# Kernel tuning notes

Hardware: AMD Instinct MI355X
Metric: run time of the kernel (lower is better)

Reference implementation:

```python
import jax, jax.numpy as jnp
import numpy as np
from jax import lax

T, B, D, H, C = 2048, 64, 128, 256, 5

def setup_inputs() -> dict:
    key = jax.random.key(0)
    k = jax.random.split(key, 7)
    s = 1.0 / np.sqrt(H)  # pytorch nn.RNN init scale
    return {
        "inputs": jax.random.normal(k[0], (T, B, D), dtype=jnp.float32),
        "W_ih": jax.random.uniform(k[1], (H, D), jnp.float32, -s, s),
        "W_hh": jax.random.uniform(k[2], (H, H), jnp.float32, -s, s),
        "b_ih": jax.random.uniform(k[3], (H,), jnp.float32, -s, s),
        "b_hh": jax.random.uniform(k[4], (H,), jnp.float32, -s, s),
        "W_fc": jax.random.uniform(k[5], (C, H), jnp.float32, -s, s),
        "b_fc": jax.random.uniform(k[6], (C,), jnp.float32, -s, s),
    }

def reference(inputs, W_ih, W_hh, b_ih, b_hh, W_fc, b_fc):
    # Precompute input projections for all timesteps: (T, B, H)
    x_proj = jnp.einsum('tbd,hd->tbh', inputs, W_ih) + b_ih + b_hh

    def step(h, xp):
        # h_t = tanh(W_ih x_t + b_ih + W_hh h_{t-1} + b_hh)
        h_new = jnp.tanh(xp + h @ W_hh.T)
        return h_new, None  # per-step outputs unused by the module head

    h0 = jnp.zeros((inputs.shape[1], W_hh.shape[0]), dtype=inputs.dtype)
    h_last, _ = lax.scan(step, h0, x_proj)

    logits = h_last @ W_fc.T + b_fc  # (B, 5)
    return jax.nn.log_softmax(logits, axis=1)
```

## Files before the change

### kernel.cpp

```cpp
#include <hip/hip_runtime.h>


#define T_DIM 2048
#define B_DIM 64
#define D_DIM 128
#define H_DIM 256
#define C_DIM 5

using floatx4 = __attribute__((ext_vector_type(4))) float;
using shortx8 = __attribute__((ext_vector_type(8))) short;

#define W_SCALE 2032.0f
#define H_SCALE 127.0f
#define INV_SCALE (1.0f / (2032.0f * 127.0f))
#define TWO_LOG2E 2.8853900817779268f
#define K_EXP (TWO_LOG2E * INV_SCALE)
#define MAGIC 12582912.0f

__device__ __forceinline__ short f2bf(float f) {
  unsigned int u = __float_as_uint(f);
  unsigned int r = (u + 0x7FFFu + ((u >> 16) & 1u)) >> 16;
  return (short)r;
}

__device__ __forceinline__ int sdot4(unsigned int a, unsigned int b, int c) {
#if __has_builtin(__builtin_amdgcn_sdot4)
  return __builtin_amdgcn_sdot4((int)a, (int)b, c, false);
#else
  int r = c;
  #pragma unroll
  for (int k = 0; k < 4; ++k)
    r += (int)(signed char)(a >> (8 * k)) * (int)(signed char)(b >> (8 * k));
  return r;
#endif
}

template<int CTRL>
__device__ __forceinline__ int dpp_movi(int x) {
  return __builtin_amdgcn_update_dpp(0, x, CTRL, 0xF, 0xF, true);
}

__device__ __forceinline__ float fast_exp2(float x) {
#if __has_builtin(__builtin_amdgcn_exp2f)
  return __builtin_amdgcn_exp2f(x);
#else
  return __exp2f(x);
#endif
}

__device__ __forceinline__ float fast_rcp(float x) {
#if __has_builtin(__builtin_amdgcn_rcpf)
  return __builtin_amdgcn_rcpf(x);
#else
  return __fdividef(1.0f, x);
#endif
}

__device__ __forceinline__ void barrier_lds_only() {
  asm volatile("s_waitcnt lgkmcnt(0)\n\ts_barrier" ::: "memory");
}

__device__ __forceinline__ void xp_body(
    const float* __restrict__ x,
    const float* __restrict__ W_ih,
    const float* __restrict__ b_ih,
    const float* __restrict__ b_hh,
    _Float16* __restrict__ xp,
    int cnt, int t0, int tstride, short* wlds)
{
  if (cnt <= 0) return;
  const int tid = threadIdx.x;
  {
    const int group = tid >> 2;
    const int sub = tid & 3;
    const int kf = group & 3;
    const int k0 = kf * 32 + sub * 8;
    #pragma unroll
    for (int i = 0; i < 16; ++i) {
      const int n = (group >> 2) * 16 + i;
      const float* src = W_ih + n * D_DIM + k0;
      float4 p0 = *(const float4*)(src);
      float4 p1 = *(const float4*)(src + 4);
      shortx8 v;
      v[0]=f2bf(p0.x); v[1]=f2bf(p0.y); v[2]=f2bf(p0.z); v[3]=f2bf(p0.w);
      v[4]=f2bf(p1.x); v[5]=f2bf(p1.y); v[6]=f2bf(p1.z); v[7]=f2bf(p1.w);
      *(shortx8*)&wlds[(group * 64 + sub * 16 + i) * 8] = v;
    }
  }
  __syncthreads();

  const int wv   = tid >> 6;
  const int lane = tid & 63;
  const int col  = lane & 15;
  const int quad = lane >> 4;

  float bias[16];
  #pragma unroll
  for (int nt = 0; nt < 16; ++nt)
    bias[nt] = b_ih[nt * 16 + col] + b_hh[nt * 16 + col];

  for (int t = t0; t < cnt; t += tstride) {
    const long m0 = (long)t * 64 + wv * 16;

    shortx8 af[4];
    const float* arow = x + (m0 + col) * D_DIM + quad * 8;
    #pragma unroll
    for (int kf = 0; kf < 4; ++kf) {
      float4 p0 = *(const float4*)(arow + kf * 32);
      float4 p1 = *(const float4*)(arow + kf * 32 + 4);
      shortx8 v;
      v[0]=f2bf(p0.x); v[1]=f2bf(p0.y); v[2]=f2bf(p0.z); v[3]=f2bf(p0.w);
      v[4]=f2bf(p1.x); v[5]=f2bf(p1.y); v[6]=f2bf(p1.z); v[7]=f2bf(p1.w);
      af[kf] = v;
    }

    #pragma unroll
    for (int nt = 0; nt < 16; ++nt) {
      floatx4 acc = {0.f, 0.f, 0.f, 0.f};
      #pragma unroll
      for (int kf = 0; kf < 4; ++kf) {
        shortx8 bfrag = *(const shortx8*)&wlds[((nt * 4 + kf) * 64 + lane) * 8];
        acc = __builtin_amdgcn_mfma_f32_16x16x32_bf16(af[kf], bfrag, acc, 0, 0, 0);
      }
      const int n = nt * 16 + col;
      #pragma unroll
      for (int r = 0; r < 4; ++r) {
        const long m = m0 + quad * 4 + r;
        xp[m * H_DIM + n] = (_Float16)(acc[r] + bias[nt]);
      }
    }
  }
}

__global__ __launch_bounds__(256) void xp_kernel(
    const float* __restrict__ x, const float* __restrict__ W_ih,
    const float* __restrict__ b_ih, const float* __restrict__ b_hh,
    _Float16* __restrict__ xp, int cnt)
{
  __shared__ __align__(16) short wlds[32768];
  xp_body(x, W_ih, b_ih, b_hh, xp, cnt, blockIdx.x, gridDim.x, wlds);
}

__global__ __launch_bounds__(256)
__attribute__((amdgpu_waves_per_eu(1, 1)))
void fused_kernel(
    const _Float16* __restrict__ xp,
    const float* __restrict__ W_hh,
    const float* __restrict__ W_fc,
    const float* __restrict__ b_fc,
    signed char* __restrict__ h8,
    float* __restrict__ out,
    int cnt, int first, int last,
    const float* __restrict__ x_next,
    const float* __restrict__ W_ih,
    const float* __restrict__ b_ih,
    const float* __restrict__ b_hh,
    _Float16* __restrict__ xp_next,
    int next_cnt)
{
  __shared__ __align__(16) short wlds[32768];
  __shared__ __align__(16) signed char hbuf[2][256];
  __shared__ float hfin[H_DIM];
  __shared__ float scratch[192];

  if (blockIdx.x >= 64) {
    xp_body(x_next, W_ih, b_ih, b_hh, xp_next, next_cnt,
            (int)blockIdx.x - 64, (int)gridDim.x - 64, wlds);
    return;
  }

  const int b   = blockIdx.x;
  const int tid = threadIdx.x;
  const int g   = tid >> 2;
  const int c   = tid & 3;

  unsigned int wq[4][16];
  const float* wbase = W_hh + (g * 4) * H_DIM + c * 64;
  #pragma unroll
  for (int r = 0; r < 4; ++r)
    #pragma unroll
    for (int i = 0; i < 16; ++i) {
      float4 f = *(const float4*)(wbase + r * H_DIM + i * 4);
      unsigned int q0 = (unsigned int)(int)rintf(f.x * W_SCALE) & 0xFFu;
      unsigned int q1 = (unsigned int)(int)rintf(f.y * W_SCALE) & 0xFFu;
      unsigned int q2 = (unsigned int)(int)rintf(f.z * W_SCALE) & 0xFFu;
      unsigned int q3 = (unsigned int)(int)rintf(f.w * W_SCALE) & 0xFFu;
      wq[r][i] = q0 | (q1 << 8) | (q2 << 16) | (q3 << 24);
    }
  #pragma unroll
  for (int r = 0; r < 4; ++r)
    #pragma unroll
    for (int i = 0; i < 16; ++i)
      asm volatile("" : "+v"(wq[r][i]));

  const int row_w = tid;
  hbuf[0][row_w] = first ? (signed char)0 : h8[b * H_DIM + row_w];
  __syncthreads();

  const size_t BH = (size_t)B_DIM * H_DIM;
  const _Float16* xpp = xp + (size_t)b * H_DIM + row_w;
  float hnlast = 0.f;

  auto step_body = [&](int bufsel, _Float16 xin) -> void {
    float xin2 = (float)xin * TWO_LOG2E;
    const signed char* hb = hbuf[bufsel] + c * 64;
    uint4 u0 = *(const uint4*)(hb);
    uint4 u1 = *(const uint4*)(hb + 16);
    uint4 u2 = *(const uint4*)(hb + 32);
    uint4 u3 = *(const uint4*)(hb + 48);
    const unsigned int hv[16] = {u0.x, u0.y, u0.z, u0.w, u1.x, u1.y, u1.z, u1.w,
                                 u2.x, u2.y, u2.z, u2.w, u3.x, u3.y, u3.z, u3.w};
    int a0l = 0, a1l = 0, a2l = 0, a3l = 0;
    int a0h = 0, a1h = 0, a2h = 0, a3h = 0;
    #pragma unroll
    for (int i = 0; i < 8; ++i) {
      a0l = sdot4(wq[0][i], hv[i], a0l);
      a1l = sdot4(wq[1][i], hv[i], a1l);
      a2l = sdot4(wq[2][i], hv[i], a2l);
      a3l = sdot4(wq[3][i], hv[i], a3l);
    }
    #pragma unroll
    for (int i = 8; i < 16; ++i) {
      a0h = sdot4(wq[0][i], hv[i], a0h);
      a1h = sdot4(wq[1][i], hv[i], a1h);
      a2h = sdot4(wq[2][i], hv[i], a2h);
      a3h = sdot4(wq[3][i], hv[i], a3h);
    }
    int a0 = a0l + a0h, a1 = a1l + a1h, a2 = a2l + a2h, a3 = a3l + a3h;
    int k01 = (c & 1) ? a1 : a0;
    int s01 = (c & 1) ? a0 : a1;
    int m0  = k01 + dpp_movi<0xB1>(s01);
    int k23 = (c & 1) ? a3 : a2;
    int s23 = (c & 1) ? a2 : a3;
    int m1  = k23 + dpp_movi<0xB1>(s23);
    int kk = (c & 2) ? m1 : m0;
    int sn = (c & 2) ? m0 : m1;
    int vi = kk + dpp_movi<0x4E>(sn);

    float arg = __builtin_fmaf((float)vi, K_EXP, xin2);
    float e   = fast_exp2(arg);
    float r   = fast_rcp(e + 1.0f);
    hnlast    = __builtin_fmaf(-254.0f, r, 127.0f);
    float qb  = __builtin_fmaf(-254.0f, r, MAGIC + 127.0f);
    hbuf[bufsel ^ 1][row_w] = (signed char)__float_as_int(qb);
    barrier_lds_only();
  };

  if ((cnt & 1) == 0 && cnt >= 2) {
    const _Float16* p = xpp;
    _Float16 x0 = p[0];
    _Float16 x1 = p[BH];
    for (int s = 0; s + 2 < cnt; s += 2) {
      step_body(0, x0); x0 = p[2 * BH];
      step_body(1, x1); x1 = p[3 * BH];
      p += 2 * BH;
    }
    step_body(0, x0);
    step_body(1, x1);
  } else {
    for (int s = 0; s < cnt; ++s)
      step_body(s & 1, xpp[(size_t)s * BH]);
  }

  h8[b * H_DIM + row_w] = hbuf[cnt & 1][row_w];

  if (last) {
    hfin[row_w] = hnlast * (1.0f / 127.0f);
    __syncthreads();
    if (tid < 160) {
      const int c5 = tid >> 5, i = tid & 31;
      float pp = 0.f;
      #pragma unroll
      for (int jj = 0; jj < 8; ++jj) {
        const int j = i * 8 + jj;
        pp += W_fc[c5 * H_DIM + j] * hfin[j];
      }
      scratch[tid] = pp;
    }
    __syncthreads();
    if (tid < C_DIM) {
      float l = b_fc[tid];
      for (int i = 0; i < 32; ++i) l += scratch[tid * 32 + i];
      scratch[160 + tid] = l;
    }
    __syncthreads();
    if (tid == 0) {
      float mx = scratch[160];
      for (int i = 1; i < C_DIM; ++i) mx = fmaxf(mx, scratch[160 + i]);
      float se = 0.f;
      for (int i = 0; i < C_DIM; ++i) se += __expf(scratch[160 + i] - mx);
      const float lse = mx + __logf(se);
      for (int i = 0; i < C_DIM; ++i) out[b * C_DIM + i] = scratch[160 + i] - lse;
    }
  }
}

extern "C" void kernel_launch(void* const* d_in, const int* in_sizes, int n_in,
                              void* d_out, int out_size, void* d_ws, size_t ws_size,
                              hipStream_t stream) {
  (void)in_sizes; (void)n_in; (void)out_size;
  const float* x    = (const float*)d_in[0];
  const float* W_ih = (const float*)d_in[1];
  const float* W_hh = (const float*)d_in[2];
  const float* b_ih = (const float*)d_in[3];
  const float* b_hh = (const float*)d_in[4];
  const float* W_fc = (const float*)d_in[5];
  const float* b_fc = (const float*)d_in[6];
  float* out = (float*)d_out;

  char* ws = (char*)d_ws;
  signed char* h8 = (signed char*)ws;
  _Float16* bufA = (_Float16*)(ws + 65536);
  const size_t step_bytes = (size_t)B_DIM * H_DIM * sizeof(_Float16);
  const size_t avail = ws_size > 65536 ? ws_size - 65536 : 0;
  const long cap2 = (long)(avail / (2 * step_bytes));

  if (cap2 >= 64) {
    long CAP = cap2 < 512 ? cap2 : 512;
    _Float16* bufB = bufA + (size_t)CAP * B_DIM * H_DIM;
    long bnd[64];
    bnd[0] = 0;
    long c0 = 256; if (c0 > CAP) c0 = CAP; if (c0 > T_DIM) c0 = T_DIM;
    bnd[1] = c0;
    int nc = 1;
    while (bnd[nc] < T_DIM && nc < 62) {
      long nx = bnd[nc] + CAP; if (nx > T_DIM) nx = T_DIM;
      bnd[nc + 1] = nx; ++nc;
    }
    {
      const unsigned gb = (unsigned)(c0 < 512 ? c0 : 512);
      xp_kernel<<<dim3(gb), dim3(256), 0, stream>>>(x, W_ih, b_ih, b_hh, bufA, (int)c0);
    }
    for (int k = 0; k < nc; ++k) {
      _Float16* src = (k & 1) ? bufB : bufA;
      _Float16* dst = (k & 1) ? bufA : bufB;
      const long s0 = bnd[k], s1 = bnd[k + 1];
      const int has_next = (k + 1 < nc) ? 1 : 0;
      const long n0 = has_next ? bnd[k + 1] : 0;
      const long n1 = has_next ? bnd[k + 2] : 0;
      fused_kernel<<<dim3(256), dim3(256), 0, stream>>>(
          src, W_hh, W_fc, b_fc, h8, out,
          (int)(s1 - s0), k == 0 ? 1 : 0, (k == nc - 1) ? 1 : 0,
          x + n0 * B_DIM * D_DIM, W_ih, b_ih, b_hh, dst, (int)(n1 - n0));
    }
  } else {
    long Tc = (long)(avail / step_bytes);
    if (Tc > T_DIM) Tc = T_DIM;
    if (Tc < 1) Tc = 1;
    for (long t0 = 0; t0 < T_DIM; t0 += Tc) {
      const long cnt = (T_DIM - t0 < Tc) ? (T_DIM - t0) : Tc;
      const unsigned gb = (unsigned)(cnt < 512 ? cnt : 512);
      xp_kernel<<<dim3(gb), dim3(256), 0, stream>>>(
          x + t0 * B_DIM * D_DIM, W_ih, b_ih, b_hh, bufA, (int)cnt);
      fused_kernel<<<dim3(64), dim3(256), 0, stream>>>(
          bufA, W_hh, W_fc, b_fc, h8, out,
          (int)cnt, t0 == 0 ? 1 : 0, (t0 + cnt == T_DIM) ? 1 : 0,
          x, W_ih, b_ih, b_hh, bufA, 0);
    }
  }
}
```

Measured before the change: 731.2 us.

## Process two batch rows per recurrent block to amortize barriers

Each recurrent block now handles two independent batch sequences, interleaving their per-step dot products before a single LDS barrier, so the barrier and latency cost per step is shared across two rows and the two chains can hide each other's latency. Recurrent blocks drop from 64 to 32, which frees more CUs for the overlapped input-projection work. The trade-off is roughly twice the serial arithmetic per block per step, which lengthens the critical path if the step was compute-bound rather than latency-bound.

```diff
diff --git a/kernel.cpp b/kernel.cpp
--- a/kernel.cpp
+++ b/kernel.cpp
@@ -159,17 +159,17 @@
     int next_cnt)
 {
   __shared__ __align__(16) short wlds[32768];
-  __shared__ __align__(16) signed char hbuf[2][256];
+  __shared__ __align__(16) signed char hbuf[2][2][256];
   __shared__ float hfin[H_DIM];
   __shared__ float scratch[192];
 
-  if (blockIdx.x >= 64) {
+  if (blockIdx.x >= 32) {
     xp_body(x_next, W_ih, b_ih, b_hh, xp_next, next_cnt,
-            (int)blockIdx.x - 64, (int)gridDim.x - 64, wlds);
+            (int)blockIdx.x - 32, (int)gridDim.x - 32, wlds);
     return;
   }
 
-  const int b   = blockIdx.x;
+  const int b0  = blockIdx.x * 2;
   const int tid = threadIdx.x;
   const int g   = tid >> 2;
   const int c   = tid & 3;
@@ -194,16 +194,18 @@
       asm volatile("" : "+v"(wq[r][i]));
 
   const int row_w = tid;
-  hbuf[0][row_w] = first ? (signed char)0 : h8[b * H_DIM + row_w];
+  hbuf[0][0][row_w] = first ? (signed char)0 : h8[b0 * H_DIM + row_w];
+  hbuf[1][0][row_w] = first ? (signed char)0 : h8[(b0 + 1) * H_DIM + row_w];
   __syncthreads();
 
   const size_t BH = (size_t)B_DIM * H_DIM;
-  const _Float16* xpp = xp + (size_t)b * H_DIM + row_w;
-  float hnlast = 0.f;
-
-  auto step_body = [&](int bufsel, _Float16 xin) -> void {
+  const _Float16* pA = xp + (size_t)b0 * H_DIM + row_w;
+  const _Float16* pB = pA + H_DIM;
+  float hn[2] = {0.f, 0.f};
+
+  auto phase = [&](int bb, int bufsel, _Float16 xin) -> void {
     float xin2 = (float)xin * TWO_LOG2E;
-    const signed char* hb = hbuf[bufsel] + c * 64;
+    const signed char* hb = hbuf[bb][bufsel] + c * 64;
     uint4 u0 = *(const uint4*)(hb);
     uint4 u1 = *(const uint4*)(hb + 16);
     uint4 u2 = *(const uint4*)(hb + 32);
@@ -240,57 +242,72 @@
     float arg = __builtin_fmaf((float)vi, K_EXP, xin2);
     float e   = fast_exp2(arg);
     float r   = fast_rcp(e + 1.0f);
-    hnlast    = __builtin_fmaf(-254.0f, r, 127.0f);
+    hn[bb]    = __builtin_fmaf(-254.0f, r, 127.0f);
     float qb  = __builtin_fmaf(-254.0f, r, MAGIC + 127.0f);
-    hbuf[bufsel ^ 1][row_w] = (signed char)__float_as_int(qb);
+    hbuf[bb][bufsel ^ 1][row_w] = (signed char)__float_as_int(qb);
+  };
+
+  if ((cnt & 1) == 0 && cnt >= 4) {
+    _Float16 xA0 = pA[0];
+    _Float16 xB0 = pB[0];
+    _Float16 xA1 = pA[BH];
+    _Float16 xB1 = pB[BH];
+    for (int s = 0; s + 2 < cnt; s += 2) {
+      phase(0, 0, xA0); phase(1, 0, xB0);
+      barrier_lds_only();
+      xA0 = pA[2 * BH]; xB0 = pB[2 * BH];
+      phase(0, 1, xA1); phase(1, 1, xB1);
+      barrier_lds_only();
+      xA1 = pA[3 * BH]; xB1 = pB[3 * BH];
+      pA += 2 * BH; pB += 2 * BH;
+    }
+    phase(0, 0, xA0); phase(1, 0, xB0);
     barrier_lds_only();
-  };
-
-  if ((cnt & 1) == 0 && cnt >= 2) {
-    const _Float16* p = xpp;
-    _Float16 x0 = p[0];
-    _Float16 x1 = p[BH];
-    for (int s = 0; s + 2 < cnt; s += 2) {
-      step_body(0, x0); x0 = p[2 * BH];
-      step_body(1, x1); x1 = p[3 * BH];
-      p += 2 * BH;
-    }
-    step_body(0, x0);
-    step_body(1, x1);
+    phase(0, 1, xA1); phase(1, 1, xB1);
+    barrier_lds_only();
   } else {
-    for (int s = 0; s < cnt; ++s)
-      step_body(s & 1, xpp[(size_t)s * BH]);
-  }
-
-  h8[b * H_DIM + row_w] = hbuf[cnt & 1][row_w];
+    for (int s = 0; s < cnt; ++s) {
+      phase(0, s & 1, pA[(size_t)s * BH]);
+      phase(1, s & 1, pB[(size_t)s * BH]);
+      barrier_lds_only();
+    }
+  }
+
+  h8[b0 * H_DIM + row_w]       = hbuf[0][cnt & 1][row_w];
+  h8[(b0 + 1) * H_DIM + row_w] = hbuf[1][cnt & 1][row_w];
 
   if (last) {
-    hfin[row_w] = hnlast * (1.0f / 127.0f);
-    __syncthreads();
-    if (tid < 160) {
-      const int c5 = tid >> 5, i = tid & 31;
-      float pp = 0.f;
-      #pragma unroll
-      for (int jj = 0; jj < 8; ++jj) {
-        const int j = i * 8 + jj;
-        pp += W_fc[c5 * H_DIM + j] * hfin[j];
-      }
-      scratch[tid] = pp;
-    }
-    __syncthreads();
-    if (tid < C_DIM) {
-      float l = b_fc[tid];
-      for (int i = 0; i < 32; ++i) l += scratch[tid * 32 + i];
-      scratch[160 + tid] = l;
-    }
-    __syncthreads();
-    if (tid == 0) {
-      float mx = scratch[160];
-      for (int i = 1; i < C_DIM; ++i) mx = fmaxf(mx, scratch[160 + i]);
-      float se = 0.f;
-      for (int i = 0; i < C_DIM; ++i) se += __expf(scratch[160 + i] - mx);
-      const float lse = mx + __logf(se);
-      for (int i = 0; i < C_DIM; ++i) out[b * C_DIM + i] = scratch[160 + i] - lse;
+    #pragma unroll
+    for (int bb = 0; bb < 2; ++bb) {
+      __syncthreads();
+      hfin[row_w] = hn[bb] * (1.0f / 127.0f);
+      __syncthreads();
+      if (tid < 160) {
+        const int c5 = tid >> 5, i = tid & 31;
+        float pp = 0.f;
+        #pragma unroll
+        for (int jj = 0; jj < 8; ++jj) {
+          const int j = i * 8 + jj;
+          pp += W_fc[c5 * H_DIM + j] * hfin[j];
+        }
+        scratch[tid] = pp;
+      }
+      __syncthreads();
+      if (tid < C_DIM) {
+        float l = b_fc[tid];
+        for (int i = 0; i < 32; ++i) l += scratch[tid * 32 + i];
+        scratch[160 + tid] = l;
+      }
+      __syncthreads();
+      if (tid == 0) {
+        float mx = scratch[160];
+        for (int i = 1; i < C_DIM; ++i) mx = fmaxf(mx, scratch[160 + i]);
+        float se = 0.f;
+        for (int i = 0; i < C_DIM; ++i) se += __expf(scratch[160 + i] - mx);
+        const float lse = mx + __logf(se);
+        for (int i = 0; i < C_DIM; ++i)
+          out[(b0 + bb) * C_DIM + i] = scratch[160 + i] - lse;
+      }
     }
   }
 }
@@ -352,7 +369,7 @@
       const unsigned gb = (unsigned)(cnt < 512 ? cnt : 512);
       xp_kernel<<<dim3(gb), dim3(256), 0, stream>>>(
           x + t0 * B_DIM * D_DIM, W_ih, b_ih, b_hh, bufA, (int)cnt);
-      fused_kernel<<<dim3(64), dim3(256), 0, stream>>>(
+      fused_kernel<<<dim3(32), dim3(256), 0, stream>>>(
           bufA, W_hh, W_fc, b_fc, h8, out,
           (int)cnt, t0 == 0 ? 1 : 0, (t0 + cnt == T_DIM) ? 1 : 0,
           x, W_ih, b_ih, b_hh, bufA, 0);
```

Result: slower. 1.189 ms (+62.6%).

## Replace chunked kernel launches with persistent cooperative producer-consumer kernel

Applied to the files above, without the earlier changes.

Replaces the sequence of per-chunk fused launches with a single cooperative persistent kernel. 192 producer blocks compute input projections into a ring buffer and publish per-chunk counters with atomics, while 64 consumer blocks spin on those flags and run the recurrence over 128-step chunks. The aim is to remove repeated launch overhead, repeated W_hh quantisation, and h8 spill/reload between chunks, and to overlap projection work with the scan. The cost is spin-wait polling and fences, and the design depends on cooperative launch co-residency, with the old multi-launch path kept as a fallback.

```diff
diff --git a/kernel.cpp b/kernel.cpp
--- a/kernel.cpp
+++ b/kernel.cpp
@@ -6,12 +6,14 @@
 #define D_DIM 128
 #define H_DIM 256
 #define C_DIM 5
+#define CHUNK 128
+#define NCH   (T_DIM / CHUNK)
+#define NPROD 192
 
 using floatx4 = __attribute__((ext_vector_type(4))) float;
 using shortx8 = __attribute__((ext_vector_type(8))) short;
 
 #define W_SCALE 2032.0f
-#define H_SCALE 127.0f
 #define INV_SCALE (1.0f / (2032.0f * 127.0f))
 #define TWO_LOG2E 2.8853900817779268f
 #define K_EXP (TWO_LOG2E * INV_SCALE)
@@ -60,122 +62,123 @@
   asm volatile("s_waitcnt lgkmcnt(0)\n\ts_barrier" ::: "memory");
 }
 
-__device__ __forceinline__ void xp_body(
-    const float* __restrict__ x,
-    const float* __restrict__ W_ih,
-    const float* __restrict__ b_ih,
-    const float* __restrict__ b_hh,
-    _Float16* __restrict__ xp,
-    int cnt, int t0, int tstride, short* wlds)
+__device__ __forceinline__ void xp_stage_w(const float* __restrict__ W_ih, short* wlds) {
+  const int tid = threadIdx.x;
+  const int group = tid >> 2;
+  const int sub = tid & 3;
+  const int kf = group & 3;
+  const int k0 = kf * 32 + sub * 8;
+  #pragma unroll
+  for (int i = 0; i < 16; ++i) {
+    const int n = (group >> 2) * 16 + i;
+    const float* src = W_ih + n * D_DIM + k0;
+    float4 p0 = *(const float4*)(src);
+    float4 p1 = *(const float4*)(src + 4);
+    shortx8 v;
+    v[0]=f2bf(p0.x); v[1]=f2bf(p0.y); v[2]=f2bf(p0.z); v[3]=f2bf(p0.w);
+    v[4]=f2bf(p1.x); v[5]=f2bf(p1.y); v[6]=f2bf(p1.z); v[7]=f2bf(p1.w);
+    *(shortx8*)&wlds[(group * 64 + sub * 16 + i) * 8] = v;
+  }
+}
+
+__device__ __forceinline__ void xp_one_t(
+    const float* __restrict__ x, const float* bias, const short* wlds,
+    long t, _Float16* __restrict__ dst)
 {
-  if (cnt <= 0) return;
-  const int tid = threadIdx.x;
-  {
-    const int group = tid >> 2;
-    const int sub = tid & 3;
-    const int kf = group & 3;
-    const int k0 = kf * 32 + sub * 8;
-    #pragma unroll
-    for (int i = 0; i < 16; ++i) {
-      const int n = (group >> 2) * 16 + i;
-      const float* src = W_ih + n * D_DIM + k0;
-      float4 p0 = *(const float4*)(src);
-      float4 p1 = *(const float4*)(src + 4);
-      shortx8 v;
-      v[0]=f2bf(p0.x); v[1]=f2bf(p0.y); v[2]=f2bf(p0.z); v[3]=f2bf(p0.w);
-      v[4]=f2bf(p1.x); v[5]=f2bf(p1.y); v[6]=f2bf(p1.z); v[7]=f2bf(p1.w);
-      *(shortx8*)&wlds[(group * 64 + sub * 16 + i) * 8] = v;
-    }
-  }
-  __syncthreads();
-
+  const int tid  = threadIdx.x;
   const int wv   = tid >> 6;
   const int lane = tid & 63;
   const int col  = lane & 15;
   const int quad = lane >> 4;
 
-  float bias[16];
-  #pragma unroll
-  for (int nt = 0; nt < 16; ++nt)
-    bias[nt] = b_ih[nt * 16 + col] + b_hh[nt * 16 + col];
-
-  for (int t = t0; t < cnt; t += tstride) {
-    const long m0 = (long)t * 64 + wv * 16;
-
-    shortx8 af[4];
-    const float* arow = x + (m0 + col) * D_DIM + quad * 8;
+  shortx8 af[4];
+  const float* arow = x + ((size_t)t * B_DIM + wv * 16 + col) * D_DIM + quad * 8;
+  #pragma unroll
+  for (int kf = 0; kf < 4; ++kf) {
+    float4 p0 = *(const float4*)(arow + kf * 32);
+    float4 p1 = *(const float4*)(arow + kf * 32 + 4);
+    shortx8 v;
+    v[0]=f2bf(p0.x); v[1]=f2bf(p0.y); v[2]=f2bf(p0.z); v[3]=f2bf(p0.w);
+    v[4]=f2bf(p1.x); v[5]=f2bf(p1.y); v[6]=f2bf(p1.z); v[7]=f2bf(p1.w);
+    af[kf] = v;
+  }
+
+  #pragma unroll
+  for (int nt = 0; nt < 16; ++nt) {
+    floatx4 acc = {0.f, 0.f, 0.f, 0.f};
     #pragma unroll
     for (int kf = 0; kf < 4; ++kf) {
-      float4 p0 = *(const float4*)(arow + kf * 32);
-      float4 p1 = *(const float4*)(arow + kf * 32 + 4);
-      shortx8 v;
-      v[0]=f2bf(p0.x); v[1]=f2bf(p0.y); v[2]=f2bf(p0.z); v[3]=f2bf(p0.w);
-      v[4]=f2bf(p1.x); v[5]=f2bf(p1.y); v[6]=f2bf(p1.z); v[7]=f2bf(p1.w);
-      af[kf] = v;
-    }
-
-    #pragma unroll
-    for (int nt = 0; nt < 16; ++nt) {
-      floatx4 acc = {0.f, 0.f, 0.f, 0.f};
-      #pragma unroll
-      for (int kf = 0; kf < 4; ++kf) {
-        shortx8 bfrag = *(const shortx8*)&wlds[((nt * 4 + kf) * 64 + lane) * 8];
-        acc = __builtin_amdgcn_mfma_f32_16x16x32_bf16(af[kf], bfrag, acc, 0, 0, 0);
-      }
-      const int n = nt * 16 + col;
-      #pragma unroll
-      for (int r = 0; r < 4; ++r) {
-        const long m = m0 + quad * 4 + r;
-        xp[m * H_DIM + n] = (_Float16)(acc[r] + bias[nt]);
-      }
-    }
-  }
-}
-
-__global__ __launch_bounds__(256) void xp_kernel(
-    const float* __restrict__ x, const float* __restrict__ W_ih,
-    const float* __restrict__ b_ih, const float* __restrict__ b_hh,
-    _Float16* __restrict__ xp, int cnt)
-{
-  __shared__ __align__(16) short wlds[32768];
-  xp_body(x, W_ih, b_ih, b_hh, xp, cnt, blockIdx.x, gridDim.x, wlds);
+      shortx8 bfrag = *(const shortx8*)&wlds[((nt * 4 + kf) * 64 + lane) * 8];
+      acc = __builtin_amdgcn_mfma_f32_16x16x32_bf16(af[kf], bfrag, acc, 0, 0, 0);
+    }
+    const int n = nt * 16 + col;
+    #pragma unroll
+    for (int r = 0; r < 4; ++r) {
+      const int m = wv * 16 + quad * 4 + r;
+      dst[(size_t)m * H_DIM + n] = (_Float16)(acc[r] + bias[nt]);
+    }
+  }
 }
 
 __global__ __launch_bounds__(256)
 __attribute__((amdgpu_waves_per_eu(1, 1)))
-void fused_kernel(
-    const _Float16* __restrict__ xp,
+void rnn_persistent(
+    const float* __restrict__ x,
+    const float* __restrict__ W_ih,
     const float* __restrict__ W_hh,
+    const float* __restrict__ b_ih,
+    const float* __restrict__ b_hh,
     const float* __restrict__ W_fc,
     const float* __restrict__ b_fc,
-    signed char* __restrict__ h8,
+    _Float16* __restrict__ ring,
+    int* __restrict__ flags,
     float* __restrict__ out,
-    int cnt, int first, int last,
-    const float* __restrict__ x_next,
-    const float* __restrict__ W_ih,
-    const float* __restrict__ b_ih,
-    const float* __restrict__ b_hh,
-    _Float16* __restrict__ xp_next,
-    int next_cnt)
+    int R)
 {
   __shared__ __align__(16) short wlds[32768];
   __shared__ __align__(16) signed char hbuf[2][256];
   __shared__ float hfin[H_DIM];
   __shared__ float scratch[192];
 
+  const int tid = threadIdx.x;
+  const size_t BH = (size_t)B_DIM * H_DIM;
+
   if (blockIdx.x >= 64) {
-    xp_body(x_next, W_ih, b_ih, b_hh, xp_next, next_cnt,
-            (int)blockIdx.x - 64, (int)gridDim.x - 64, wlds);
+    xp_stage_w(W_ih, wlds);
+    const int lane = tid & 63, col = lane & 15;
+    float bias[16];
+    #pragma unroll
+    for (int nt = 0; nt < 16; ++nt)
+      bias[nt] = b_ih[nt * 16 + col] + b_hh[nt * 16 + col];
+    __syncthreads();
+
+    const int pidx = (int)blockIdx.x - 64;
+    for (int t = pidx; t < T_DIM; t += NPROD) {
+      const int c = t >> 7;
+      if (c >= R) {
+        if (tid == 0) {
+          while (__hip_atomic_load(&flags[16], __ATOMIC_RELAXED,
+                                   __HIP_MEMORY_SCOPE_AGENT) < 64 * (c - R + 1)) {}
+        }
+        __syncthreads();
+      }
+      _Float16* dst = ring + ((size_t)(c % R) * CHUNK + (t & (CHUNK - 1))) * BH;
+      xp_one_t(x, bias, wlds, t, dst);
+      __threadfence();
+      __syncthreads();
+      if (tid == 0)
+        __hip_atomic_fetch_add(&flags[c], 1, __ATOMIC_RELEASE,
+                               __HIP_MEMORY_SCOPE_AGENT);
+    }
     return;
   }
 
-  const int b   = blockIdx.x;
-  const int tid = threadIdx.x;
-  const int g   = tid >> 2;
-  const int c   = tid & 3;
+  const int b = blockIdx.x;
+  const int g = tid >> 2;
+  const int c4 = tid & 3;
 
   unsigned int wq[4][16];
-  const float* wbase = W_hh + (g * 4) * H_DIM + c * 64;
+  const float* wbase = W_hh + (g * 4) * H_DIM + c4 * 64;
   #pragma unroll
   for (int r = 0; r < 4; ++r)
     #pragma unroll
@@ -194,16 +197,14 @@
       asm volatile("" : "+v"(wq[r][i]));
 
   const int row_w = tid;
-  hbuf[0][row_w] = first ? (signed char)0 : h8[b * H_DIM + row_w];
+  hbuf[0][row_w] = 0;
   __syncthreads();
 
-  const size_t BH = (size_t)B_DIM * H_DIM;
-  const _Float16* xpp = xp + (size_t)b * H_DIM + row_w;
   float hnlast = 0.f;
 
   auto step_body = [&](int bufsel, _Float16 xin) -> void {
-    float xin2 = (float)xin * TWO_LOG2E;
-    const signed char* hb = hbuf[bufsel] + c * 64;
+    float x2 = (float)xin * TWO_LOG2E;
+    const signed char* hb = hbuf[bufsel] + c4 * 64;
     uint4 u0 = *(const uint4*)(hb);
     uint4 u1 = *(const uint4*)(hb + 16);
     uint4 u2 = *(const uint4*)(hb + 32);
@@ -227,17 +228,184 @@
       a3h = sdot4(wq[3][i], hv[i], a3h);
     }
     int a0 = a0l + a0h, a1 = a1l + a1h, a2 = a2l + a2h, a3 = a3l + a3h;
-    int k01 = (c & 1) ? a1 : a0;
-    int s01 = (c & 1) ? a0 : a1;
+    int k01 = (c4 & 1) ? a1 : a0;
+    int s01 = (c4 & 1) ? a0 : a1;
     int m0  = k01 + dpp_movi<0xB1>(s01);
-    int k23 = (c & 1) ? a3 : a2;
-    int s23 = (c & 1) ? a2 : a3;
+    int k23 = (c4 & 1) ? a3 : a2;
+    int s23 = (c4 & 1) ? a2 : a3;
     int m1  = k23 + dpp_movi<0xB1>(s23);
-    int kk = (c & 2) ? m1 : m0;
-    int sn = (c & 2) ? m0 : m1;
+    int kk = (c4 & 2) ? m1 : m0;
+    int sn = (c4 & 2) ? m0 : m1;
     int vi = kk + dpp_movi<0x4E>(sn);
 
-    float arg = __builtin_fmaf((float)vi, K_EXP, xin2);
+    float arg = __builtin_fmaf((float)vi, K_EXP, x2);
+    float e   = fast_exp2(arg);
+    float r   = fast_rcp(e + 1.0f);
+    hnlast    = __builtin_fmaf(-254.0f, r, 127.0f);
+    float qb  = __builtin_fmaf(-254.0f, r, MAGIC + 127.0f);
+    hbuf[bufsel ^ 1][row_w] = (signed char)__float_as_int(qb);
+    barrier_lds_only();
+  };
+
+  for (int c = 0; c < NCH; ++c) {
+    if (tid == 0) {
+      while (__hip_atomic_load(&flags[c], __ATOMIC_RELAXED,
+                               __HIP_MEMORY_SCOPE_AGENT) < CHUNK) {}
+    }
+    __syncthreads();
+    {
+      int fv = __hip_atomic_load(&flags[c], __ATOMIC_ACQUIRE,
+                                 __HIP_MEMORY_SCOPE_AGENT);
+      asm volatile("" :: "v"(fv));
+    }
+
+    const _Float16* p = ring + (size_t)(c % R) * CHUNK * BH
+                             + (size_t)b * H_DIM + row_w;
+    _Float16 x0 = p[0];
+    _Float16 x1 = p[BH];
+    for (int s = 0; s + 2 < CHUNK; s += 2) {
+      step_body(0, x0); x0 = p[2 * BH];
+      step_body(1, x1); x1 = p[3 * BH];
+      p += 2 * BH;
+    }
+    step_body(0, x0);
+    step_body(1, x1);
+
+    if (R < NCH) {
+      __syncthreads();
+      if (tid == 0)
+        __hip_atomic_fetch_add(&flags[16], 1, __ATOMIC_RELAXED,
+                               __HIP_MEMORY_SCOPE_AGENT);
+    }
+  }
+
+  hfin[row_w] = hnlast * (1.0f / 127.0f);
+  __syncthreads();
+  if (tid < 160) {
+    const int c5 = tid >> 5, i = tid & 31;
+    float pp = 0.f;
+    #pragma unroll
+    for (int jj = 0; jj < 8; ++jj) {
+      const int j = i * 8 + jj;
+      pp += W_fc[c5 * H_DIM + j] * hfin[j];
+    }
+    scratch[tid] = pp;
+  }
+  __syncthreads();
+  if (tid < C_DIM) {
+    float l = b_fc[tid];
+    for (int i = 0; i < 32; ++i) l += scratch[tid * 32 + i];
+    scratch[160 + tid] = l;
+  }
+  __syncthreads();
+  if (tid == 0) {
+    float mx = scratch[160];
+    for (int i = 1; i < C_DIM; ++i) mx = fmaxf(mx, scratch[160 + i]);
+    float se = 0.f;
+    for (int i = 0; i < C_DIM; ++i) se += __expf(scratch[160 + i] - mx);
+    const float lse = mx + __logf(se);
+    for (int i = 0; i < C_DIM; ++i) out[b * C_DIM + i] = scratch[160 + i] - lse;
+  }
+}
+
+__global__ __launch_bounds__(256) void xp_fb_kernel(
+    const float* __restrict__ x, const float* __restrict__ W_ih,
+    const float* __restrict__ b_ih, const float* __restrict__ b_hh,
+    _Float16* __restrict__ xp, int cnt)
+{
+  __shared__ __align__(16) short wlds[32768];
+  if (cnt <= 0) return;
+  xp_stage_w(W_ih, wlds);
+  const int col = (threadIdx.x & 63) & 15;
+  float bias[16];
+  #pragma unroll
+  for (int nt = 0; nt < 16; ++nt)
+    bias[nt] = b_ih[nt * 16 + col] + b_hh[nt * 16 + col];
+  __syncthreads();
+  for (int t = blockIdx.x; t < cnt; t += gridDim.x)
+    xp_one_t(x, bias, wlds, t, xp + (size_t)t * B_DIM * H_DIM);
+}
+
+__global__ __launch_bounds__(256)
+__attribute__((amdgpu_waves_per_eu(1, 1)))
+void scan_fb_kernel(
+    const _Float16* __restrict__ xp, const float* __restrict__ W_hh,
+    const float* __restrict__ W_fc, const float* __restrict__ b_fc,
+    signed char* __restrict__ h8, float* __restrict__ out,
+    int cnt, int first, int last)
+{
+  __shared__ __align__(16) signed char hbuf[2][256];
+  __shared__ float hfin[H_DIM];
+  __shared__ float scratch[192];
+  const int b = blockIdx.x;
+  const int tid = threadIdx.x;
+  const int g = tid >> 2;
+  const int c4 = tid & 3;
+
+  unsigned int wq[4][16];
+  const float* wbase = W_hh + (g * 4) * H_DIM + c4 * 64;
+  #pragma unroll
+  for (int r = 0; r < 4; ++r)
+    #pragma unroll
+    for (int i = 0; i < 16; ++i) {
+      float4 f = *(const float4*)(wbase + r * H_DIM + i * 4);
+      unsigned int q0 = (unsigned int)(int)rintf(f.x * W_SCALE) & 0xFFu;
+      unsigned int q1 = (unsigned int)(int)rintf(f.y * W_SCALE) & 0xFFu;
+      unsigned int q2 = (unsigned int)(int)rintf(f.z * W_SCALE) & 0xFFu;
+      unsigned int q3 = (unsigned int)(int)rintf(f.w * W_SCALE) & 0xFFu;
+      wq[r][i] = q0 | (q1 << 8) | (q2 << 16) | (q3 << 24);
+    }
+  #pragma unroll
+  for (int r = 0; r < 4; ++r)
+    #pragma unroll
+    for (int i = 0; i < 16; ++i)
+      asm volatile("" : "+v"(wq[r][i]));
+
+  const int row_w = tid;
+  hbuf[0][row_w] = first ? (signed char)0 : h8[b * H_DIM + row_w];
+  __syncthreads();
+
+  const size_t BH = (size_t)B_DIM * H_DIM;
+  const _Float16* xpp = xp + (size_t)b * H_DIM + row_w;
+  float hnlast = 0.f;
+
+  auto step_body = [&](int bufsel, _Float16 xin) -> void {
+    float x2 = (float)xin * TWO_LOG2E;
+    const signed char* hb = hbuf[bufsel] + c4 * 64;
+    uint4 u0 = *(const uint4*)(hb);
+    uint4 u1 = *(const uint4*)(hb + 16);
+    uint4 u2 = *(const uint4*)(hb + 32);
+    uint4 u3 = *(const uint4*)(hb + 48);
+    const unsigned int hv[16] = {u0.x, u0.y, u0.z, u0.w, u1.x, u1.y, u1.z, u1.w,
+                                 u2.x, u2.y, u2.z, u2.w, u3.x, u3.y, u3.z, u3.w};
+    int a0l = 0, a1l = 0, a2l = 0, a3l = 0;
+    int a0h = 0, a1h = 0, a2h = 0, a3h = 0;
+    #pragma unroll
+    for (int i = 0; i < 8; ++i) {
+      a0l = sdot4(wq[0][i], hv[i], a0l);
+      a1l = sdot4(wq[1][i], hv[i], a1l);
+      a2l = sdot4(wq[2][i], hv[i], a2l);
+      a3l = sdot4(wq[3][i], hv[i], a3l);
+    }
+    #pragma unroll
+    for (int i = 8; i < 16; ++i) {
+      a0h = sdot4(wq[0][i], hv[i], a0h);
+      a1h = sdot4(wq[1][i], hv[i], a1h);
+      a2h = sdot4(wq[2][i], hv[i], a2h);
+      a3h = sdot4(wq[3][i], hv[i], a3h);
+    }
+    int a0 = a0l + a0h, a1 = a1l + a1h, a2 = a2l + a2h, a3 = a3l + a3h;
+    int k01 = (c4 & 1) ? a1 : a0;
+    int s01 = (c4 & 1) ? a0 : a1;
+    int m0  = k01 + dpp_movi<0xB1>(s01);
+    int k23 = (c4 & 1) ? a3 : a2;
+    int s23 = (c4 & 1) ? a2 : a3;
+    int m1  = k23 + dpp_movi<0xB1>(s23);
+    int kk = (c4 & 2) ? m1 : m0;
+    int sn = (c4 & 2) ? m0 : m1;
+    int vi = kk + dpp_movi<0x4E>(sn);
+
+    float arg = __builtin_fmaf((float)vi, K_EXP, x2);
     float e   = fast_exp2(arg);
     float r   = fast_rcp(e + 1.0f);
     hnlast    = __builtin_fmaf(-254.0f, r, 127.0f);
@@ -309,53 +477,39 @@
   float* out = (float*)d_out;
 
   char* ws = (char*)d_ws;
-  signed char* h8 = (signed char*)ws;
-  _Float16* bufA = (_Float16*)(ws + 65536);
+  int* flags = (int*)ws;
+  _Float16* ring = (_Float16*)(ws + 65536);
   const size_t step_bytes = (size_t)B_DIM * H_DIM * sizeof(_Float16);
   const size_t avail = ws_size > 65536 ? ws_size - 65536 : 0;
-  const long cap2 = (long)(avail / (2 * step_bytes));
-
-  if (cap2 >= 64) {
-    long CAP = cap2 < 512 ? cap2 : 512;
-    _Float16* bufB = bufA + (size_t)CAP * B_DIM * H_DIM;
-    long bnd[64];
-    bnd[0] = 0;
-    long c0 = 256; if (c0 > CAP) c0 = CAP; if (c0 > T_DIM) c0 = T_DIM;
-    bnd[1] = c0;
-    int nc = 1;
-    while (bnd[nc] < T_DIM && nc < 62) {
-      long nx = bnd[nc] + CAP; if (nx > T_DIM) nx = T_DIM;
-      bnd[nc + 1] = nx; ++nc;
-    }
-    {
-      const unsigned gb = (unsigned)(c0 < 512 ? c0 : 512);
-      xp_kernel<<<dim3(gb), dim3(256), 0, stream>>>(x, W_ih, b_ih, b_hh, bufA, (int)c0);
-    }
-    for (int k = 0; k < nc; ++k) {
-      _Float16* src = (k & 1) ? bufB : bufA;
-      _Float16* dst = (k & 1) ? bufA : bufB;
-      const long s0 = bnd[k], s1 = bnd[k + 1];
-      const int has_next = (k + 1 < nc) ? 1 : 0;
-      const long n0 = has_next ? bnd[k + 1] : 0;
-      const long n1 = has_next ? bnd[k + 2] : 0;
-      fused_kernel<<<dim3(256), dim3(256), 0, stream>>>(
-          src, W_hh, W_fc, b_fc, h8, out,
-          (int)(s1 - s0), k == 0 ? 1 : 0, (k == nc - 1) ? 1 : 0,
-          x + n0 * B_DIM * D_DIM, W_ih, b_ih, b_hh, dst, (int)(n1 - n0));
-    }
-  } else {
-    long Tc = (long)(avail / step_bytes);
-    if (Tc > T_DIM) Tc = T_DIM;
-    if (Tc < 1) Tc = 1;
-    for (long t0 = 0; t0 < T_DIM; t0 += Tc) {
-      const long cnt = (T_DIM - t0 < Tc) ? (T_DIM - t0) : Tc;
-      const unsigned gb = (unsigned)(cnt < 512 ? cnt : 512);
-      xp_kernel<<<dim3(gb), dim3(256), 0, stream>>>(
-          x + t0 * B_DIM * D_DIM, W_ih, b_ih, b_hh, bufA, (int)cnt);
-      fused_kernel<<<dim3(64), dim3(256), 0, stream>>>(
-          bufA, W_hh, W_fc, b_fc, h8, out,
-          (int)cnt, t0 == 0 ? 1 : 0, (t0 + cnt == T_DIM) ? 1 : 0,
-          x, W_ih, b_ih, b_hh, bufA, 0);
-    }
-  }
-}
+  const long steps = (long)(avail / step_bytes);
+
+  int Rv = (int)(steps / CHUNK);
+  if (Rv > NCH) Rv = NCH;
+
+  if (Rv >= 2) {
+    hipMemsetAsync(ws, 0, 256, stream);
+    void* args[11];
+    args[0] = (void*)&x;    args[1] = (void*)&W_ih; args[2] = (void*)&W_hh;
+    args[3] = (void*)&b_ih; args[4] = (void*)&b_hh; args[5] = (void*)&W_fc;
+    args[6] = (void*)&b_fc; args[7] = (void*)&ring; args[8] = (void*)&flags;
+    args[9] = (void*)&out;  args[10] = (void*)&Rv;
+    hipError_t e = hipLaunchCooperativeKernel(
+        (const void*)rnn_persistent, dim3(256), dim3(256), args, 0, stream);
+    if (e == hipSuccess) return;
+  }
+
+  signed char* h8 = (signed char*)(ws + 4096);
+  long Tc = steps;
+  if (Tc > T_DIM) Tc = T_DIM;
+  if (Tc >= 2) Tc &= ~1L;
+  if (Tc < 1) Tc = 1;
+  for (long t0 = 0; t0 < T_DIM; t0 += Tc) {
+    const long cnt = (T_DIM - t0 < Tc) ? (T_DIM - t0) : Tc;
+    const unsigned gb = (unsigned)(cnt < 512 ? cnt : 512);
+    xp_fb_kernel<<<dim3(gb), dim3(256), 0, stream>>>(
+        x + t0 * B_DIM * D_DIM, W_ih, b_ih, b_hh, ring, (int)cnt);
+    scan_fb_kernel<<<dim3(64), dim3(256), 0, stream>>>(
+        ring, W_hh, W_fc, b_fc, h8, out,
+        (int)cnt, t0 == 0 ? 1 : 0, (t0 + cnt == T_DIM) ? 1 : 0);
+  }
+}
```

New measurement: 1.000 ms. 1.37x slower.
